# Optimization experiments

Hardware: AMD Instinct MI355X
Metric: run time of the kernel (lower is better)

## Reference

```python
import jax, jax.numpy as jnp
import numpy as np

N, L, CS, CZ, CH, H = 1, 768, 384, 128, 32, 12
EPS = 1e-5


def _layernorm(x, w, b):
    m = jnp.mean(x, axis=-1, keepdims=True)
    v = jnp.mean((x - m) ** 2, axis=-1, keepdims=True)
    return (x - m) * jax.lax.rsqrt(v + EPS) * w + b


def setup_inputs() -> dict:
    key = jax.random.key(0)
    ks = jax.random.split(key, 12)
    scale = 0.02
    return {
        "s": jax.random.normal(ks[0], (N, L, CS), jnp.float32),
        "z": jax.random.normal(ks[1], (N, L, L, CZ), jnp.float32),
        "ln_s_w": jnp.ones((CS,), jnp.float32),
        "ln_s_b": jnp.zeros((CS,), jnp.float32),
        "ln_z_w": jnp.ones((CZ,), jnp.float32),
        "ln_z_b": jnp.zeros((CZ,), jnp.float32),
        "w_z": jax.random.normal(ks[2], (H, CZ), jnp.float32) * scale,   # pair-bias proj (no bias)
        "w_q": jax.random.normal(ks[3], (H * CH, CS), jnp.float32) * scale,
        "w_k": jax.random.normal(ks[4], (H * CH, CS), jnp.float32) * scale,
        "w_v": jax.random.normal(ks[5], (H * CH, CS), jnp.float32) * scale,
        "w_g": jax.random.normal(ks[6], (H * CH, CS), jnp.float32) * scale,
        "b_g": jnp.zeros((H * CH,), jnp.float32),
        "w_o": jax.random.normal(ks[7], (CS, H * CH), jnp.float32) * scale,
        "b_o": jnp.zeros((CS,), jnp.float32),
    }


def reference(s, z, ln_s_w, ln_s_b, ln_z_w, ln_z_b, w_z, w_q, w_k, w_v, w_g, b_g, w_o, b_o):
    s_n = _layernorm(s, ln_s_w, ln_s_b)            # [N,L,CS]
    z_n = _layernorm(z, ln_z_w, ln_z_b)            # [N,L,L,CZ]
    # pair bias: Linear(c_z -> H, bias=False), then permute to [N,H,L,L]
    bias = jnp.einsum("nijc,hc->nhij", z_n, w_z)   # [N,H,L,L]
    # AF2-style gated MHA on s
    q = jnp.einsum("nlc,dc->nld", s_n, w_q).reshape(N, L, H, CH) * (CH ** -0.5)
    k = jnp.einsum("nlc,dc->nld", s_n, w_k).reshape(N, L, H, CH)
    v = jnp.einsum("nlc,dc->nld", s_n, w_v).reshape(N, L, H, CH)
    logits = jnp.einsum("nqhc,nkhc->nhqk", q, k) + bias
    a = jax.nn.softmax(logits, axis=-1)
    o = jnp.einsum("nhqk,nkhc->nqhc", a, v).reshape(N, L, H * CH)
    g = jax.nn.sigmoid(jnp.einsum("nlc,dc->nld", s_n, w_g) + b_g)
    o = o * g
    return jnp.einsum("nld,cd->nlc", o, w_o) + b_o  # [N,L,CS]
```

## Files before the change

kernel.cpp:

```cpp
#include <hip/hip_runtime.h>
#include <hip/hip_bf16.h>
#include <cstddef>

#define L_ 768
#define CS_ 384
#define CZ_ 128
#define CH_ 32
#define H_ 12
#define LL_ (L_*L_)
#define EPS_ 1e-5f

typedef float f4 __attribute__((ext_vector_type(4)));
typedef float f2 __attribute__((ext_vector_type(2)));

__global__ void prep_kernel(const float* __restrict__ lnzw, const float* __restrict__ lnzb,
                            const float* __restrict__ wz,
                            float* __restrict__ ww, float* __restrict__ sumww,
                            float* __restrict__ bb) {
    int t = threadIdx.x;
    int h = t >> 4;
    int c0 = (t & 15) * 8;
    if (h < H_) {
        float sw = 0.f, sb = 0.f;
        #pragma unroll
        for (int c = c0; c < c0 + 8; ++c) {
            float wv = lnzw[c] * wz[h*CZ_ + c];
            ww[h*CZ_ + c] = wv;
            sw += wv;
            sb += lnzb[c] * wz[h*CZ_ + c];
        }
        #pragma unroll
        for (int off = 8; off; off >>= 1) {
            sw += __shfl_xor(sw, off);
            sb += __shfl_xor(sb, off);
        }
        if ((t & 15) == 0) { sumww[h] = sw; bb[h] = sb; }
    }
}

__global__ __launch_bounds__(128) void bias_kernel(const float* __restrict__ z,
        const float* __restrict__ ww, const float* __restrict__ sumww,
        const float* __restrict__ bb, float* __restrict__ bias) {
    __shared__ float zb[2][256*36];
    __shared__ float lw[H_*CZ_];
    __shared__ float lsw[H_];
    __shared__ float lbb[H_];

    const int t  = threadIdx.x;
    const size_t tb = (size_t)blockIdx.x * 256;
    const int sr = t >> 3;
    const int s8 = t & 7;
    const int rg = t & 63;
    const int hg = t >> 6;

    const f4* zf4 = (const f4*)z;

    f4 st[16];
    #pragma unroll
    for (int p = 0; p < 16; ++p)
        st[p] = __builtin_nontemporal_load(&zf4[(tb + p*16 + sr)*32 + s8]);

    {
        const f4* wwf4 = (const f4*)ww;
        f4* lwf4 = (f4*)lw;
        #pragma unroll
        for (int i = 0; i < 3; ++i) lwf4[i*128 + t] = wwf4[i*128 + t];
        if (t < H_) { lsw[t] = sumww[t]; lbb[t] = bb[t]; }
    }

    float acc[6][4];
    #pragma unroll
    for (int h = 0; h < 6; ++h)
        #pragma unroll
        for (int i = 0; i < 4; ++i) acc[h][i] = 0.f;
    float sm[4] = {0,0,0,0}, sq[4] = {0,0,0,0};

    #pragma unroll 1
    for (int c = 0; c < 4; ++c) {
        #pragma unroll
        for (int p = 0; p < 16; ++p) {
            const int wr = p*16 + sr;
            const int wsl = (wr >> 2) + 64*(wr & 3);
            *(f4*)&zb[c&1][wsl*36 + s8*4] = st[p];
        }
        if (c < 3) {
            #pragma unroll
            for (int p = 0; p < 16; ++p)
                st[p] = __builtin_nontemporal_load(&zf4[(tb + p*16 + sr)*32 + (c+1)*8 + s8]);
        }
        __syncthreads();

        #pragma unroll
        for (int j = 0; j < 8; ++j) {
            f4 zv[4];
            #pragma unroll
            for (int i = 0; i < 4; ++i)
                zv[i] = *(const f4*)&zb[c&1][(rg + 64*i)*36 + j*4];
            #pragma unroll
            for (int i = 0; i < 4; ++i) {
                sm[i] += zv[i].x + zv[i].y + zv[i].z + zv[i].w;
                sq[i] += zv[i].x*zv[i].x + zv[i].y*zv[i].y + zv[i].z*zv[i].z + zv[i].w*zv[i].w;
            }
            const int cb = c*32 + j*4;
            #pragma unroll
            for (int h = 0; h < 6; ++h) {
                f4 wv = *(const f4*)&lw[(hg*6 + h)*CZ_ + cb];
                #pragma unroll
                for (int i = 0; i < 4; ++i)
                    acc[h][i] += zv[i].x*wv.x + zv[i].y*wv.y + zv[i].z*wv.z + zv[i].w*wv.w;
            }
        }
        __syncthreads();
    }

    float mm[4], rr[4];
    #pragma unroll
    for (int i = 0; i < 4; ++i) {
        mm[i] = sm[i] * (1.f/CZ_);
        rr[i] = rsqrtf(sq[i]*(1.f/CZ_) - mm[i]*mm[i] + EPS_);
    }
    #pragma unroll
    for (int h = 0; h < 6; ++h) {
        const int hh = hg*6 + h;
        const float sw = lsw[hh], bbv = lbb[hh];
        f4 o;
        o.x = rr[0]*(acc[h][0] - mm[0]*sw) + bbv;
        o.y = rr[1]*(acc[h][1] - mm[1]*sw) + bbv;
        o.z = rr[2]*(acc[h][2] - mm[2]*sw) + bbv;
        o.w = rr[3]*(acc[h][3] - mm[3]*sw) + bbv;
        *(f4*)(bias + (size_t)hh*LL_ + tb + rg*4) = o;
    }
}

__global__ void sln_kernel(const float* __restrict__ s, const float* __restrict__ w,
                           const float* __restrict__ b, float* __restrict__ sn) {
    int row = blockIdx.x;
    int lane = threadIdx.x;
    float x[6];
    float sum = 0.f, sum2 = 0.f;
    #pragma unroll
    for (int j = 0; j < 6; ++j) {
        x[j] = s[row*CS_ + lane + j*64];
        sum += x[j]; sum2 += x[j]*x[j];
    }
    #pragma unroll
    for (int off = 32; off; off >>= 1) {
        sum  += __shfl_xor(sum,  off);
        sum2 += __shfl_xor(sum2, off);
    }
    float m = sum * (1.f/CS_);
    float r = rsqrtf(sum2*(1.f/CS_) - m*m + EPS_);
    #pragma unroll
    for (int j = 0; j < 6; ++j) {
        int c = lane + j*64;
        sn[row*CS_ + c] = (x[j]-m)*r*w[c] + b[c];
    }
}

__global__ __launch_bounds__(256) void qkvg_kernel(const float* __restrict__ sn,
        const float* __restrict__ wq, const float* __restrict__ wk,
        const float* __restrict__ wv, const float* __restrict__ wg,
        const float* __restrict__ bg,
        float* __restrict__ qb, float* __restrict__ kb,
        float* __restrict__ vb, float* __restrict__ gb) {
    __shared__ float As[16][68];
    __shared__ float Bs[16][68];
    int m0 = blockIdx.x * 64;
    int n0 = blockIdx.y * 64;
    int sel = n0 / 384;
    const float* W = (sel==0) ? wq : (sel==1) ? wk : (sel==2) ? wv : wg;
    float* C       = (sel==0) ? qb : (sel==1) ? kb : (sel==2) ? vb : gb;
    int ncol0 = n0 - sel*384;

    int t  = threadIdx.x;
    int lr = t >> 2;
    int lc = (t & 3) * 4;
    int ty = t >> 4;
    int tx = t & 15;

    float acc[4][4] = {};
    for (int k0 = 0; k0 < CS_; k0 += 16) {
        float4 av = *(const float4*)(sn + (size_t)(m0 + lr)*CS_ + k0 + lc);
        float4 bv = *(const float4*)(W  + (size_t)(ncol0 + lr)*CS_ + k0 + lc);
        As[lc+0][lr] = av.x; As[lc+1][lr] = av.y; As[lc+2][lr] = av.z; As[lc+3][lr] = av.w;
        Bs[lc+0][lr] = bv.x; Bs[lc+1][lr] = bv.y; Bs[lc+2][lr] = bv.z; Bs[lc+3][lr] = bv.w;
        __syncthreads();
        #pragma unroll
        for (int kk = 0; kk < 16; ++kk) {
            float4 a4 = *(const float4*)&As[kk][ty*4];
            float4 b4 = *(const float4*)&Bs[kk][tx*4];
            float a[4] = {a4.x,a4.y,a4.z,a4.w};
            float bb_[4] = {b4.x,b4.y,b4.z,b4.w};
            #pragma unroll
            for (int i = 0; i < 4; ++i)
                #pragma unroll
                for (int j = 0; j < 4; ++j)
                    acc[i][j] += a[i]*bb_[j];
        }
        __syncthreads();
    }
    #pragma unroll
    for (int i = 0; i < 4; ++i) {
        int row = m0 + ty*4 + i;
        #pragma unroll
        for (int j = 0; j < 4; ++j) {
            int col = ncol0 + tx*4 + j;
            float v = acc[i][j];
            if (sel == 0) v *= 0.17677669529663687f;
            if (sel == 3) v = 1.f/(1.f + __expf(-(v + bg[col])));
            C[(size_t)row*CS_ + col] = v;
        }
    }
}

#define QT_ 8
__global__ __launch_bounds__(256) void attn_kernel(const float* __restrict__ qb,
        const float* __restrict__ kb, const float* __restrict__ vb,
        const float* __restrict__ gb, const float* __restrict__ bias,
        float* __restrict__ og) {
    __shared__ float Sm[QT_][772];
    __shared__ float KVt[CH_][136];
    int h  = blockIdx.x;
    int q0 = blockIdx.y * QT_;
    int t  = threadIdx.x;

    int tq = t >> 5;
    int tk = t & 31;

    float qreg[CH_];
    {
        const float4* qsrc = (const float4*)(qb + (size_t)(q0 + tq)*CS_ + h*CH_);
        #pragma unroll
        for (int i = 0; i < 8; ++i) {
            float4 qv = qsrc[i];
            qreg[i*4+0]=qv.x; qreg[i*4+1]=qv.y; qreg[i*4+2]=qv.z; qreg[i*4+3]=qv.w;
        }
    }

    for (int kt = 0; kt < L_; kt += 128) {
        #pragma unroll
        for (int r2 = 0; r2 < 4; ++r2) {
            int row = (t >> 3) + 32*r2;
            int c   = (t & 7) * 4;
            f4 kv = *(const f4*)(kb + (size_t)(kt+row)*CS_ + h*CH_ + c);
            KVt[c+0][row]=kv.x; KVt[c+1][row]=kv.y; KVt[c+2][row]=kv.z; KVt[c+3][row]=kv.w;
        }
        __syncthreads();
        f4 sacc = {0,0,0,0};
        #pragma unroll
        for (int c = 0; c < CH_; ++c) {
            f4 kv4 = *(const f4*)&KVt[c][tk*4];
            sacc.x += qreg[c]*kv4.x;
            sacc.y += qreg[c]*kv4.y;
            sacc.z += qreg[c]*kv4.z;
            sacc.w += qreg[c]*kv4.w;
        }
        f4 bv = *(const f4*)(bias + (size_t)h*LL_ + (size_t)(q0+tq)*L_ + kt + tk*4);
        *(f4*)&Sm[tq][kt + tk*4] = sacc + bv;
        __syncthreads();
    }

    {
        float mx = -1e30f;
        for (int k = tk; k < L_; k += 32) mx = fmaxf(mx, Sm[tq][k]);
        #pragma unroll
        for (int off = 16; off; off >>= 1) mx = fmaxf(mx, __shfl_xor(mx, off));
        float ssum = 0.f;
        for (int k = tk; k < L_; k += 32) {
            float e = __expf(Sm[tq][k] - mx);
            Sm[tq][k] = e;
            ssum += e;
        }
        #pragma unroll
        for (int off = 16; off; off >>= 1) ssum += __shfl_xor(ssum, off);
        float inv = 1.f/ssum;
        for (int k = tk; k < L_; k += 32) Sm[tq][k] *= inv;
        __syncthreads();
    }

    {
        float o = 0.f;
        for (int kt = 0; kt < L_; kt += 128) {
            #pragma unroll
            for (int r2 = 0; r2 < 4; ++r2) {
                int row = (t >> 3) + 32*r2;
                int c   = (t & 7) * 4;
                f4 vv = *(const f4*)(vb + (size_t)(kt+row)*CS_ + h*CH_ + c);
                KVt[c+0][row]=vv.x; KVt[c+1][row]=vv.y; KVt[c+2][row]=vv.z; KVt[c+3][row]=vv.w;
            }
            __syncthreads();
            #pragma unroll
            for (int j4 = 0; j4 < 32; ++j4) {
                f4 pv = *(const f4*)&Sm[tq][kt + j4*4];
                f4 va = *(const f4*)&KVt[tk][j4*4];
                o += pv.x*va.x + pv.y*va.y + pv.z*va.z + pv.w*va.w;
            }
            __syncthreads();
        }
        int row = q0 + tq;
        int c   = h*CH_ + tk;
        og[(size_t)row*CS_ + c] = o * gb[(size_t)row*CS_ + c];
    }
}

__global__ __launch_bounds__(256) void outproj_kernel(const float* __restrict__ og,
        const float* __restrict__ wo, const float* __restrict__ bo,
        float* __restrict__ out) {
    __shared__ float As[16][36];
    __shared__ float Bs[16][36];
    int m0 = blockIdx.x * 32;
    int n0 = blockIdx.y * 32;
    int t  = threadIdx.x;
    int lr = t >> 3;
    int lc = (t & 7) * 2;
    int ty = t >> 4;
    int tx = t & 15;
    float acc[2][2] = {};
    for (int k0 = 0; k0 < CS_; k0 += 16) {
        f2 av = *(const f2*)(og + (size_t)(m0 + lr)*CS_ + k0 + lc);
        f2 bv = *(const f2*)(wo + (size_t)(n0 + lr)*CS_ + k0 + lc);
        As[lc+0][lr] = av.x; As[lc+1][lr] = av.y;
        Bs[lc+0][lr] = bv.x; Bs[lc+1][lr] = bv.y;
        __syncthreads();
        #pragma unroll
        for (int kk = 0; kk < 16; ++kk) {
            f2 a2 = *(const f2*)&As[kk][ty*2];
            f2 b2 = *(const f2*)&Bs[kk][tx*2];
            acc[0][0] += a2.x*b2.x;
            acc[0][1] += a2.x*b2.y;
            acc[1][0] += a2.y*b2.x;
            acc[1][1] += a2.y*b2.y;
        }
        __syncthreads();
    }
    #pragma unroll
    for (int i = 0; i < 2; ++i) {
        int row = m0 + ty*2 + i;
        #pragma unroll
        for (int j = 0; j < 2; ++j) {
            int col = n0 + tx*2 + j;
            out[(size_t)row*CS_ + col] = acc[i][j] + bo[col];
        }
    }
}

extern "C" void kernel_launch(void* const* d_in, const int* in_sizes, int n_in,
                              void* d_out, int out_size, void* d_ws, size_t ws_size,
                              hipStream_t stream) {
    const float* s      = (const float*)d_in[0];
    const float* z      = (const float*)d_in[1];
    const float* ln_s_w = (const float*)d_in[2];
    const float* ln_s_b = (const float*)d_in[3];
    const float* ln_z_w = (const float*)d_in[4];
    const float* ln_z_b = (const float*)d_in[5];
    const float* w_z    = (const float*)d_in[6];
    const float* w_q    = (const float*)d_in[7];
    const float* w_k    = (const float*)d_in[8];
    const float* w_v    = (const float*)d_in[9];
    const float* w_g    = (const float*)d_in[10];
    const float* b_g    = (const float*)d_in[11];
    const float* w_o    = (const float*)d_in[12];
    const float* b_o    = (const float*)d_in[13];
    float* out = (float*)d_out;

    float* ws    = (float*)d_ws;
    float* bias  = ws;
    float* sn    = bias + (size_t)H_*LL_;
    float* qb    = sn + (size_t)L_*CS_;
    float* kb    = qb + (size_t)L_*CS_;
    float* vb    = kb + (size_t)L_*CS_;
    float* gb    = vb + (size_t)L_*CS_;
    float* og    = gb + (size_t)L_*CS_;
    float* ww    = og + (size_t)L_*CS_;
    float* sumww = ww + (size_t)H_*CZ_;
    float* bbuf  = sumww + 16;

    hipLaunchKernelGGL(prep_kernel, dim3(1), dim3(256), 0, stream,
                       ln_z_w, ln_z_b, w_z, ww, sumww, bbuf);
    hipLaunchKernelGGL(bias_kernel, dim3(LL_/256), dim3(128), 0, stream,
                       z, ww, sumww, bbuf, bias);
    hipLaunchKernelGGL(sln_kernel, dim3(L_), dim3(64), 0, stream,
                       s, ln_s_w, ln_s_b, sn);
    hipLaunchKernelGGL(qkvg_kernel, dim3(L_/64, 1536/64), dim3(256), 0, stream,
                       sn, w_q, w_k, w_v, w_g, b_g, qb, kb, vb, gb);
    hipLaunchKernelGGL(attn_kernel, dim3(H_, L_/QT_), dim3(256), 0, stream,
                       qb, kb, vb, gb, bias, og);
    hipLaunchKernelGGL(outproj_kernel, dim3(L_/32, CS_/32), dim3(256), 0, stream,
                       og, w_o, b_o, out);
}
```

Measured before the change: 204.7 us.

## Simplify pair-bias kernel to one row per thread with direct global loads

Replaces the LDS-staged, double-buffered z tile (each thread computing 4 rows by 6 heads) with a design where each of 256 threads owns one pair row. Each thread loads its 128 channels directly from global memory as float4 and accumulates all 12 heads, with the weights kept in shared memory. This removes the large LDS footprint and the per-chunk barriers, which may raise occupancy. The trade-off is strided, uncoalesced per-thread row loads (512 B apart across lanes) and scalar rather than vectorized bias stores, which could hurt effective bandwidth on this bandwidth-bound kernel.

Measured after the change: 218.2 us. 1.07x slower.

```diff
diff --git a/kernel.cpp b/kernel.cpp
--- a/kernel.cpp
+++ b/kernel.cpp
@@ -38,98 +38,51 @@
     }
 }
 
-__global__ __launch_bounds__(128) void bias_kernel(const float* __restrict__ z,
+__global__ __launch_bounds__(256) void bias_kernel(const float* __restrict__ z,
         const float* __restrict__ ww, const float* __restrict__ sumww,
         const float* __restrict__ bb, float* __restrict__ bias) {
-    __shared__ float zb[2][256*36];
     __shared__ float lw[H_*CZ_];
     __shared__ float lsw[H_];
     __shared__ float lbb[H_];
 
-    const int t  = threadIdx.x;
-    const size_t tb = (size_t)blockIdx.x * 256;
-    const int sr = t >> 3;
-    const int s8 = t & 7;
-    const int rg = t & 63;
-    const int hg = t >> 6;
-
-    const f4* zf4 = (const f4*)z;
-
-    f4 st[16];
-    #pragma unroll
-    for (int p = 0; p < 16; ++p)
-        st[p] = __builtin_nontemporal_load(&zf4[(tb + p*16 + sr)*32 + s8]);
-
-    {
-        const f4* wwf4 = (const f4*)ww;
-        f4* lwf4 = (f4*)lw;
-        #pragma unroll
-        for (int i = 0; i < 3; ++i) lwf4[i*128 + t] = wwf4[i*128 + t];
-        if (t < H_) { lsw[t] = sumww[t]; lbb[t] = bb[t]; }
-    }
-
-    float acc[6][4];
-    #pragma unroll
-    for (int h = 0; h < 6; ++h)
-        #pragma unroll
-        for (int i = 0; i < 4; ++i) acc[h][i] = 0.f;
-    float sm[4] = {0,0,0,0}, sq[4] = {0,0,0,0};
+    const int t = threadIdx.x;
+    const size_t row = (size_t)blockIdx.x * 256 + t;
+    const f4* zr = (const f4*)(z + row * CZ_);
+
+    for (int i = t; i < H_*CZ_; i += 256) lw[i] = ww[i];
+    if (t < H_) { lsw[t] = sumww[t]; lbb[t] = bb[t]; }
+
+    float acc[H_];
+    #pragma unroll
+    for (int h = 0; h < H_; ++h) acc[h] = 0.f;
+    float sm = 0.f, sq = 0.f;
+
+    __syncthreads();
 
     #pragma unroll 1
     for (int c = 0; c < 4; ++c) {
-        #pragma unroll
-        for (int p = 0; p < 16; ++p) {
-            const int wr = p*16 + sr;
-            const int wsl = (wr >> 2) + 64*(wr & 3);
-            *(f4*)&zb[c&1][wsl*36 + s8*4] = st[p];
-        }
-        if (c < 3) {
-            #pragma unroll
-            for (int p = 0; p < 16; ++p)
-                st[p] = __builtin_nontemporal_load(&zf4[(tb + p*16 + sr)*32 + (c+1)*8 + s8]);
-        }
-        __syncthreads();
-
+        f4 st[8];
+        #pragma unroll
+        for (int j = 0; j < 8; ++j) st[j] = zr[c*8 + j];
         #pragma unroll
         for (int j = 0; j < 8; ++j) {
-            f4 zv[4];
-            #pragma unroll
-            for (int i = 0; i < 4; ++i)
-                zv[i] = *(const f4*)&zb[c&1][(rg + 64*i)*36 + j*4];
-            #pragma unroll
-            for (int i = 0; i < 4; ++i) {
-                sm[i] += zv[i].x + zv[i].y + zv[i].z + zv[i].w;
-                sq[i] += zv[i].x*zv[i].x + zv[i].y*zv[i].y + zv[i].z*zv[i].z + zv[i].w*zv[i].w;
-            }
+            f4 zv = st[j];
+            sm += zv.x + zv.y + zv.z + zv.w;
+            sq += zv.x*zv.x + zv.y*zv.y + zv.z*zv.z + zv.w*zv.w;
             const int cb = c*32 + j*4;
             #pragma unroll
-            for (int h = 0; h < 6; ++h) {
-                f4 wv = *(const f4*)&lw[(hg*6 + h)*CZ_ + cb];
-                #pragma unroll
-                for (int i = 0; i < 4; ++i)
-                    acc[h][i] += zv[i].x*wv.x + zv[i].y*wv.y + zv[i].z*wv.z + zv[i].w*wv.w;
+            for (int h = 0; h < H_; ++h) {
+                f4 wv = *(const f4*)&lw[h*CZ_ + cb];
+                acc[h] += zv.x*wv.x + zv.y*wv.y + zv.z*wv.z + zv.w*wv.w;
             }
         }
-        __syncthreads();
-    }
-
-    float mm[4], rr[4];
-    #pragma unroll
-    for (int i = 0; i < 4; ++i) {
-        mm[i] = sm[i] * (1.f/CZ_);
-        rr[i] = rsqrtf(sq[i]*(1.f/CZ_) - mm[i]*mm[i] + EPS_);
-    }
-    #pragma unroll
-    for (int h = 0; h < 6; ++h) {
-        const int hh = hg*6 + h;
-        const float sw = lsw[hh], bbv = lbb[hh];
-        f4 o;
-        o.x = rr[0]*(acc[h][0] - mm[0]*sw) + bbv;
-        o.y = rr[1]*(acc[h][1] - mm[1]*sw) + bbv;
-        o.z = rr[2]*(acc[h][2] - mm[2]*sw) + bbv;
-        o.w = rr[3]*(acc[h][3] - mm[3]*sw) + bbv;
-        *(f4*)(bias + (size_t)hh*LL_ + tb + rg*4) = o;
-    }
+    }
+
+    float m = sm * (1.f/CZ_);
+    float r = rsqrtf(sq*(1.f/CZ_) - m*m + EPS_);
+    #pragma unroll
+    for (int h = 0; h < H_; ++h)
+        bias[(size_t)h*LL_ + row] = r*(acc[h] - m*lsw[h]) + lbb[h];
 }
 
 __global__ void sln_kernel(const float* __restrict__ s, const float* __restrict__ w,
@@ -377,7 +330,7 @@
 
     hipLaunchKernelGGL(prep_kernel, dim3(1), dim3(256), 0, stream,
                        ln_z_w, ln_z_b, w_z, ww, sumww, bbuf);
-    hipLaunchKernelGGL(bias_kernel, dim3(LL_/256), dim3(128), 0, stream,
+    hipLaunchKernelGGL(bias_kernel, dim3(LL_/256), dim3(256), 0, stream,
                        z, ww, sumww, bbuf, bias);
     hipLaunchKernelGGL(sln_kernel, dim3(L_), dim3(64), 0, stream,
                        s, ln_s_w, ln_s_b, sn);
```
